# Optimization experiments

Hardware: AMD Instinct MI355X
Metric: run time of the kernel (lower is better)

## Reference

```python
import jax, jax.numpy as jnp
import numpy as np

BETA_MIN = 1e-06


def setup_inputs() -> dict:
    key = jax.random.key(0)
    ks = jax.random.split(key, 4)
    B, H, W, C = 32, 56, 56, 256
    x = jax.random.normal(ks[0], (B, H, W, C), dtype=jnp.float32)
    # NonNeg-constrained weights, init value gamma_init = 1/16
    gamma_k = jax.random.uniform(ks[1], (1, 1, 8, C), dtype=jnp.float32) * (1.0 / 16.0)
    gamma_s = jax.random.uniform(ks[2], (3, 3, C, 1), dtype=jnp.float32) * (1.0 / 16.0)
    beta = jax.random.uniform(ks[3], (C,), dtype=jnp.float32) * 1e-06
    beta_outside = jnp.zeros((C,), dtype=jnp.float32)
    gamma_outside = jnp.ones((C,), dtype=jnp.float32)
    return {
        'x': x,
        'gamma_k': gamma_k,
        'gamma_s': gamma_s,
        'beta': beta,
        'beta_outside': beta_outside,
        'gamma_outside': gamma_outside,
        'surround_dist': 1,
    }


def reference(x, gamma_k, gamma_s, beta, beta_outside, gamma_outside, surround_dist):
    B, H, W, C = x.shape
    G = C // 8  # norm_groups = C / 8, 8 channels per group

    x2 = x * x

    # Grouped 1x1 conv: gamma_k[0,0] is [8, C]; group g uses columns g*8:(g+1)*8
    # reshape to [in=8, group, out=8] and contract per group.
    w = gamma_k[0, 0].reshape(8, G, 8)  # [i, g, o]
    Pk = jnp.einsum('bhwgi,igo->bhwgo', x2.reshape(B, H, W, G, 8), w)
    Pk = Pk.reshape(B, H, W, C)

    # Masked (center-zero) dilated 3x3 depthwise conv on squared inputs.
    mask = jnp.array([[1.0, 1.0, 1.0], [1.0, 0.0, 1.0], [1.0, 1.0, 1.0]], dtype=x.dtype)
    k = gamma_s[..., 0] * mask[:, :, None]  # [3, 3, C]
    kern = k[:, :, None, :]  # HWIO with I = C/groups = 1, O = C
    Ps = jax.lax.conv_general_dilated(
        x2, kern,
        window_strides=(1, 1),
        padding='SAME',
        rhs_dilation=(surround_dist, surround_dist),
        dimension_numbers=('NHWC', 'HWIO', 'NHWC'),
        feature_group_count=C,
    )

    # Divisive normalization: x / sqrt(Pk + Ps + beta + beta_min), then affine.
    norm_pool = jnp.reciprocal(jnp.sqrt(Pk + Ps + (beta + BETA_MIN)))
    return x * norm_pool * gamma_outside + beta_outside
```

## Files before the change

kernel.cpp:

```cpp
#include <hip/hip_runtime.h>

#define BB 32
#define HH 56
#define WW 56
#define CC 256
#define PSTRIP 4
#define STRIPS_PER_ROW (WW / PSTRIP)

__device__ __forceinline__ void load8(const float* __restrict__ p, float v[8]) {
    float4 a = *reinterpret_cast<const float4*>(p);
    float4 b = *reinterpret_cast<const float4*>(p + 4);
    v[0]=a.x; v[1]=a.y; v[2]=a.z; v[3]=a.w;
    v[4]=b.x; v[5]=b.y; v[6]=b.z; v[7]=b.w;
}

__global__ __launch_bounds__(256, 2) void dn_kernel(
    const float* __restrict__ x,
    const float* __restrict__ gk_g,
    const float* __restrict__ gs_g,
    const float* __restrict__ beta,
    const float* __restrict__ beta_o,
    const float* __restrict__ gamma_o,
    const int* __restrict__ sdist,
    float* __restrict__ out)
{
    const int d   = sdist[0];
    const int tid = blockIdx.x * 256 + threadIdx.x;
    const int g   = tid & 31;
    const int s   = tid >> 5;
    const int sw  = s % STRIPS_PER_ROW;
    const int t1  = s / STRIPS_PER_ROW;
    const int h   = t1 % HH;
    const int b   = t1 / HH;
    const int w0  = sw * PSTRIP;
    const int c0  = g << 3;

    float gk[8][8];
#pragma unroll
    for (int i = 0; i < 8; ++i) load8(gk_g + i*CC + c0, gk[i]);

    const int tap_kh[8] = {0,0,0,1,1,2,2,2};
    const int tap_kw[8] = {0,1,2,0,2,0,1,2};
    float gs[8][8];
#pragma unroll
    for (int t = 0; t < 8; ++t)
        load8(gs_g + (tap_kh[t]*3 + tap_kw[t])*CC + c0, gs[t]);

    float betav[8], gov[8], bov[8];
    load8(beta    + c0, betav);
    load8(gamma_o + c0, gov);
    load8(beta_o  + c0, bov);
#pragma unroll
    for (int o = 0; o < 8; ++o) betav[o] += 1e-6f;

    const float* xrow = x   + (size_t)((b*HH + h)*WW)*CC;
    float*       orow = out + (size_t)((b*HH + h)*WW)*CC;

#pragma unroll
    for (int j = 0; j < PSTRIP; ++j) {
        const int w = w0 + j;

        float cx[8];
        load8(xrow + w*CC + c0, cx);

        float acc[8];
#pragma unroll
        for (int o = 0; o < 8; ++o) acc[o] = betav[o];

#pragma unroll
        for (int i = 0; i < 8; ++i) {
            const float x2 = cx[i]*cx[i];
#pragma unroll
            for (int o = 0; o < 8; ++o) acc[o] += x2 * gk[i][o];
        }

#pragma unroll
        for (int t = 0; t < 8; ++t) {
            const int hh = h + (tap_kh[t]-1)*d;
            const int w2 = w + (tap_kw[t]-1)*d;
            if (hh >= 0 && hh < HH && w2 >= 0 && w2 < WW) {
                float xn[8];
                load8(x + (size_t)((b*HH + hh)*WW + w2)*CC + c0, xn);
#pragma unroll
                for (int o = 0; o < 8; ++o) acc[o] += (xn[o]*xn[o]) * gs[t][o];
            }
        }

        float res[8];
#pragma unroll
        for (int o = 0; o < 8; ++o) {
            const float np = __builtin_amdgcn_rsqf(acc[o]);
            res[o] = cx[o] * np * gov[o] + bov[o];
        }
        float4* op = reinterpret_cast<float4*>(orow + w*CC + c0);
        op[0] = make_float4(res[0], res[1], res[2], res[3]);
        op[1] = make_float4(res[4], res[5], res[6], res[7]);
    }
}

extern "C" void kernel_launch(void* const* d_in, const int* in_sizes, int n_in,
                              void* d_out, int out_size, void* d_ws, size_t ws_size,
                              hipStream_t stream) {
    const float* x       = (const float*)d_in[0];
    const float* gamma_k = (const float*)d_in[1];
    const float* gamma_s = (const float*)d_in[2];
    const float* beta    = (const float*)d_in[3];
    const float* beta_o  = (const float*)d_in[4];
    const float* gamma_o = (const float*)d_in[5];
    const int*   sdist   = (const int*)d_in[6];
    float* out = (float*)d_out;

    const int total  = BB * HH * STRIPS_PER_ROW * 32;
    const int blocks = total / 256;
    dn_kernel<<<blocks, 256, 0, stream>>>(x, gamma_k, gamma_s, beta,
                                          beta_o, gamma_o, sdist, out);
}
```

Before: 267.1 us.

## Stage squared input tile with halo in LDS for depthwise and grouped conv

Each block now covers an 8-row by full-width spatial tile over 16 channels. It first loads the tile plus a one-pixel halo into shared memory, squared and with the float4 slots rotated to avoid bank conflicts. The 3x3 neighbour taps and the centre grouped 1x1 conv then read squared values from LDS instead of issuing 8 redundant global loads per pixel. Block indices are also remapped so that each XCD handles distinct batches, which is meant to improve L2 locality. The halo layout is sized for dilation 1, so larger surround_dist values would read outside the staged tile, and occupancy may be limited by the ~37KB LDS allocation.

```diff
diff --git a/kernel.cpp b/kernel.cpp
--- a/kernel.cpp
+++ b/kernel.cpp
@@ -1,20 +1,27 @@
 #include <hip/hip_runtime.h>
+
+typedef float floatx4 __attribute__((ext_vector_type(4)));
 
 #define BB 32
 #define HH 56
 #define WW 56
 #define CC 256
-#define PSTRIP 4
-#define STRIPS_PER_ROW (WW / PSTRIP)
+#define TILE_H 8
+#define HTILES 7
+#define CT 16
+#define CTILES 16
+#define SROWS (TILE_H + 2)
+#define SW (WW + 2)
+#define LDS_F4 (SROWS * SW * (CT/4))
 
 __device__ __forceinline__ void load8(const float* __restrict__ p, float v[8]) {
-    float4 a = *reinterpret_cast<const float4*>(p);
-    float4 b = *reinterpret_cast<const float4*>(p + 4);
-    v[0]=a.x; v[1]=a.y; v[2]=a.z; v[3]=a.w;
-    v[4]=b.x; v[5]=b.y; v[6]=b.z; v[7]=b.w;
+    floatx4 a = *reinterpret_cast<const floatx4*>(p);
+    floatx4 b = *reinterpret_cast<const floatx4*>(p + 4);
+    v[0]=a[0]; v[1]=a[1]; v[2]=a[2]; v[3]=a[3];
+    v[4]=b[0]; v[5]=b[1]; v[6]=b[2]; v[7]=b[3];
 }
 
-__global__ __launch_bounds__(256, 2) void dn_kernel(
+__global__ __launch_bounds__(128, 2) void dn_kernel(
     const float* __restrict__ x,
     const float* __restrict__ gk_g,
     const float* __restrict__ gs_g,
@@ -24,77 +31,119 @@
     const int* __restrict__ sdist,
     float* __restrict__ out)
 {
-    const int d   = sdist[0];
-    const int tid = blockIdx.x * 256 + threadIdx.x;
-    const int g   = tid & 31;
-    const int s   = tid >> 5;
-    const int sw  = s % STRIPS_PER_ROW;
-    const int t1  = s / STRIPS_PER_ROW;
-    const int h   = t1 % HH;
-    const int b   = t1 / HH;
-    const int w0  = sw * PSTRIP;
-    const int c0  = g << 3;
+    __shared__ float x2s[SROWS * SW * CT];
+
+    const int d = sdist[0];
+
+    const int xcd = blockIdx.x & 7;
+    const int q   = blockIdx.x >> 3;
+    const int b   = xcd + ((q / (HTILES*CTILES)) << 3);
+    const int t0  = q % (HTILES*CTILES);
+    const int htile = t0 >> 4;
+    const int ctile = t0 & 15;
+    const int h0 = htile * TILE_H;
+    const int c0 = ctile * CT;
+    const int tid = threadIdx.x;
+
+    const float* xb = x + (size_t)b * HH * WW * CC;
+
+    {
+        floatx4* ls = (floatx4*)x2s;
+        for (int s = tid; s < LDS_F4; s += 128) {
+            const int c4 = s & 3;
+            const int wp = (s >> 2) % SW;
+            const int r  = s / (SW * 4);
+            const int h  = h0 - 1 + r;
+            const int w  = wp - 1;
+            floatx4 v = {0.f, 0.f, 0.f, 0.f};
+            if ((unsigned)h < HH && (unsigned)w < WW) {
+                const int src4 = (c4 - wp) & 3;
+                const floatx4* gp = (const floatx4*)(xb + (size_t)(h*WW + w)*CC + c0) + src4;
+                floatx4 u = *gp;
+                v = u * u;
+            }
+            ls[s] = v;
+        }
+    }
+
+    const int row   = tid >> 4;
+    const int strip = (tid >> 1) & 7;
+    const int gi    = tid & 1;
+    const int cb    = c0 + gi * 8;
+    const int o4a   = gi * 2, o4b = gi * 2 + 1;
 
     float gk[8][8];
 #pragma unroll
-    for (int i = 0; i < 8; ++i) load8(gk_g + i*CC + c0, gk[i]);
+    for (int i = 0; i < 8; ++i) load8(gk_g + i*CC + cb, gk[i]);
 
     const int tap_kh[8] = {0,0,0,1,1,2,2,2};
     const int tap_kw[8] = {0,1,2,0,2,0,1,2};
     float gs[8][8];
 #pragma unroll
     for (int t = 0; t < 8; ++t)
-        load8(gs_g + (tap_kh[t]*3 + tap_kw[t])*CC + c0, gs[t]);
+        load8(gs_g + (tap_kh[t]*3 + tap_kw[t])*CC + cb, gs[t]);
 
     float betav[8], gov[8], bov[8];
-    load8(beta    + c0, betav);
-    load8(gamma_o + c0, gov);
-    load8(beta_o  + c0, bov);
+    load8(beta    + cb, betav);
+    load8(gamma_o + cb, gov);
+    load8(beta_o  + cb, bov);
 #pragma unroll
     for (int o = 0; o < 8; ++o) betav[o] += 1e-6f;
 
-    const float* xrow = x   + (size_t)((b*HH + h)*WW)*CC;
-    float*       orow = out + (size_t)((b*HH + h)*WW)*CC;
+    __syncthreads();
 
-#pragma unroll
-    for (int j = 0; j < PSTRIP; ++j) {
-        const int w = w0 + j;
+    const int h = h0 + row;
+    const float* xrow = xb + (size_t)(h * WW) * CC;
+    float*       orow = out + ((size_t)(b * HH + h) * WW) * CC;
+    const floatx4* ls = (const floatx4*)x2s;
+
+    for (int j = 0; j < 7; ++j) {
+        const int w  = strip * 7 + j;
+        const int wp = w + 1;
 
         float cx[8];
-        load8(xrow + w*CC + c0, cx);
+        load8(xrow + w*CC + cb, cx);
 
         float acc[8];
 #pragma unroll
         for (int o = 0; o < 8; ++o) acc[o] = betav[o];
 
+        int t = 0;
 #pragma unroll
-        for (int i = 0; i < 8; ++i) {
-            const float x2 = cx[i]*cx[i];
+        for (int dr = -1; dr <= 1; ++dr) {
 #pragma unroll
-            for (int o = 0; o < 8; ++o) acc[o] += x2 * gk[i][o];
-        }
-
+            for (int dw = -1; dw <= 1; ++dw) {
+                const int rt = row + 1 + dr * d;
+                const int wt = wp + dw * d;
+                const int fb = (rt * SW + wt) * (CT/4);
+                const floatx4 A = ls[fb + ((o4a + wt) & 3)];
+                const floatx4 B = ls[fb + ((o4b + wt) & 3)];
+                if (dr == 0 && dw == 0) {
 #pragma unroll
-        for (int t = 0; t < 8; ++t) {
-            const int hh = h + (tap_kh[t]-1)*d;
-            const int w2 = w + (tap_kw[t]-1)*d;
-            if (hh >= 0 && hh < HH && w2 >= 0 && w2 < WW) {
-                float xn[8];
-                load8(x + (size_t)((b*HH + hh)*WW + w2)*CC + c0, xn);
+                    for (int o = 0; o < 8; ++o)
+                        acc[o] += A[0]*gk[0][o] + A[1]*gk[1][o]
+                                + A[2]*gk[2][o] + A[3]*gk[3][o]
+                                + B[0]*gk[4][o] + B[1]*gk[5][o]
+                                + B[2]*gk[6][o] + B[3]*gk[7][o];
+                } else {
 #pragma unroll
-                for (int o = 0; o < 8; ++o) acc[o] += (xn[o]*xn[o]) * gs[t][o];
+                    for (int o = 0; o < 4; ++o) acc[o]     += A[o] * gs[t][o];
+#pragma unroll
+                    for (int o = 0; o < 4; ++o) acc[4 + o] += B[o] * gs[t][4 + o];
+                    ++t;
+                }
             }
         }
 
-        float res[8];
+        floatx4 r0, r1;
 #pragma unroll
-        for (int o = 0; o < 8; ++o) {
-            const float np = __builtin_amdgcn_rsqf(acc[o]);
-            res[o] = cx[o] * np * gov[o] + bov[o];
+        for (int o = 0; o < 4; ++o) {
+            r0[o] = cx[o]     * __builtin_amdgcn_rsqf(acc[o])     * gov[o]     + bov[o];
+            r1[o] = cx[4 + o] * __builtin_amdgcn_rsqf(acc[4 + o]) * gov[4 + o] + bov[4 + o];
         }
-        float4* op = reinterpret_cast<float4*>(orow + w*CC + c0);
-        op[0] = make_float4(res[0], res[1], res[2], res[3]);
-        op[1] = make_float4(res[4], res[5], res[6], res[7]);
+        floatx4* op = (floatx4*)(orow + w*CC + cb);
+        op[0] = r0;
+        op[1] = r1;
     }
 }
 
@@ -110,8 +159,7 @@
     const int*   sdist   = (const int*)d_in[6];
     float* out = (float*)d_out;
 
-    const int total  = BB * HH * STRIPS_PER_ROW * 32;
-    const int blocks = total / 256;
-    dn_kernel<<<blocks, 256, 0, stream>>>(x, gamma_k, gamma_s, beta,
+    const int blocks = BB * HTILES * CTILES;
+    dn_kernel<<<blocks, 128, 0, stream>>>(x, gamma_k, gamma_s, beta,
                                           beta_o, gamma_o, sdist, out);
 }
```

After: 245.3 us. 8.2% less time.

## Remap threads to 4 channels each with 2D tiles and XCD-aware block mapping

Applied to the files above, without the earlier changes.

Each thread now computes 4 output channels instead of 8, so a wavefront covers a full pixel's 256 channels and a block covers a 4-row by 4-column tile. Block indices are swizzled so that each XCD works on its own images, which should improve L2 reuse of the neighbouring halo rows. The change also loads all neighbour taps before the math, uses nontemporal stores for the output and raises the occupancy hint. The trade-off is that the grouped 1x1 conv now reads the group's 8 inputs redundantly in pairs of lanes.

```diff
diff --git a/kernel.cpp b/kernel.cpp
--- a/kernel.cpp
+++ b/kernel.cpp
@@ -1,20 +1,18 @@
 #include <hip/hip_runtime.h>
+
+typedef float floatx4 __attribute__((ext_vector_type(4)));
 
 #define BB 32
 #define HH 56
 #define WW 56
 #define CC 256
 #define PSTRIP 4
-#define STRIPS_PER_ROW (WW / PSTRIP)
+#define WSTRIPS 14
+#define HTILE 4
+#define HTILES 14
+#define BLOCKS_PER_IMG (HTILES * WSTRIPS)
 
-__device__ __forceinline__ void load8(const float* __restrict__ p, float v[8]) {
-    float4 a = *reinterpret_cast<const float4*>(p);
-    float4 b = *reinterpret_cast<const float4*>(p + 4);
-    v[0]=a.x; v[1]=a.y; v[2]=a.z; v[3]=a.w;
-    v[4]=b.x; v[5]=b.y; v[6]=b.z; v[7]=b.w;
-}
-
-__global__ __launch_bounds__(256, 2) void dn_kernel(
+__global__ __launch_bounds__(256, 3) void dn_kernel(
     const float* __restrict__ x,
     const float* __restrict__ gk_g,
     const float* __restrict__ gs_g,
@@ -24,77 +22,77 @@
     const int* __restrict__ sdist,
     float* __restrict__ out)
 {
-    const int d   = sdist[0];
-    const int tid = blockIdx.x * 256 + threadIdx.x;
-    const int g   = tid & 31;
-    const int s   = tid >> 5;
-    const int sw  = s % STRIPS_PER_ROW;
-    const int t1  = s / STRIPS_PER_ROW;
-    const int h   = t1 % HH;
-    const int b   = t1 / HH;
-    const int w0  = sw * PSTRIP;
-    const int c0  = g << 3;
-
-    float gk[8][8];
-#pragma unroll
-    for (int i = 0; i < 8; ++i) load8(gk_g + i*CC + c0, gk[i]);
+    const int d    = sdist[0];
+    const int xcd  = blockIdx.x & 7;
+    const int q    = blockIdx.x >> 3;
+    const int b    = xcd + ((q / BLOCKS_PER_IMG) << 3);
+    const int t0   = q % BLOCKS_PER_IMG;
+    const int h    = (t0 / WSTRIPS) * HTILE + (threadIdx.x >> 6);
+    const int w0   = (t0 % WSTRIPS) * PSTRIP;
+    const int lane = threadIdx.x & 63;
+    const int c0   = lane << 2;
+    const int cg   = c0 & ~7;
 
     const int tap_kh[8] = {0,0,0,1,1,2,2,2};
     const int tap_kw[8] = {0,1,2,0,2,0,1,2};
-    float gs[8][8];
+
+    floatx4 gk[8];
 #pragma unroll
-    for (int t = 0; t < 8; ++t)
-        load8(gs_g + (tap_kh[t]*3 + tap_kw[t])*CC + c0, gs[t]);
+    for (int i = 0; i < 8; ++i)
+        gk[i] = *reinterpret_cast<const floatx4*>(gk_g + i*CC + c0);
 
-    float betav[8], gov[8], bov[8];
-    load8(beta    + c0, betav);
-    load8(gamma_o + c0, gov);
-    load8(beta_o  + c0, bov);
+    floatx4 gsw[8];
 #pragma unroll
-    for (int o = 0; o < 8; ++o) betav[o] += 1e-6f;
+    for (int tt = 0; tt < 8; ++tt)
+        gsw[tt] = *reinterpret_cast<const floatx4*>(
+                      gs_g + (tap_kh[tt]*3 + tap_kw[tt])*CC + c0);
 
-    const float* xrow = x   + (size_t)((b*HH + h)*WW)*CC;
-    float*       orow = out + (size_t)((b*HH + h)*WW)*CC;
+    floatx4 betav = *reinterpret_cast<const floatx4*>(beta + c0);
+    betav += 1e-6f;
+    const floatx4 gov = *reinterpret_cast<const floatx4*>(gamma_o + c0);
+    const floatx4 bov = *reinterpret_cast<const floatx4*>(beta_o  + c0);
+
+    const float* xb   = x + (size_t)b * HH * WW * CC;
+    const float* xrow = xb + (size_t)h * WW * CC;
+    float*       orow = out + ((size_t)(b*HH + h) * WW) * CC;
 
 #pragma unroll
     for (int j = 0; j < PSTRIP; ++j) {
         const int w = w0 + j;
+        const float* cp = xrow + w*CC;
 
-        float cx[8];
-        load8(xrow + w*CC + c0, cx);
+        floatx4 cxa = *reinterpret_cast<const floatx4*>(cp + cg);
+        floatx4 cxb = *reinterpret_cast<const floatx4*>(cp + cg + 4);
 
-        float acc[8];
+        floatx4 tp[8];
 #pragma unroll
-        for (int o = 0; o < 8; ++o) acc[o] = betav[o];
-
-#pragma unroll
-        for (int i = 0; i < 8; ++i) {
-            const float x2 = cx[i]*cx[i];
-#pragma unroll
-            for (int o = 0; o < 8; ++o) acc[o] += x2 * gk[i][o];
+        for (int tt = 0; tt < 8; ++tt) {
+            const int hh = h + (tap_kh[tt]-1)*d;
+            const int w2 = w + (tap_kw[tt]-1)*d;
+            floatx4 v = {0.f, 0.f, 0.f, 0.f};
+            if ((unsigned)hh < HH && (unsigned)w2 < WW)
+                v = *reinterpret_cast<const floatx4*>(
+                        xb + (size_t)(hh*WW + w2)*CC + c0);
+            tp[tt] = v;
         }
 
+        floatx4 acc = betav;
+        const floatx4 sqa = cxa*cxa, sqb = cxb*cxb;
 #pragma unroll
-        for (int t = 0; t < 8; ++t) {
-            const int hh = h + (tap_kh[t]-1)*d;
-            const int w2 = w + (tap_kw[t]-1)*d;
-            if (hh >= 0 && hh < HH && w2 >= 0 && w2 < WW) {
-                float xn[8];
-                load8(x + (size_t)((b*HH + hh)*WW + w2)*CC + c0, xn);
+        for (int i = 0; i < 4; ++i) acc += sqa[i] * gk[i];
 #pragma unroll
-                for (int o = 0; o < 8; ++o) acc[o] += (xn[o]*xn[o]) * gs[t][o];
-            }
-        }
+        for (int i = 0; i < 4; ++i) acc += sqb[i] * gk[4+i];
+#pragma unroll
+        for (int tt = 0; tt < 8; ++tt) acc += (tp[tt]*tp[tt]) * gsw[tt];
 
-        float res[8];
+        const floatx4 cxo = (lane & 1) ? cxb : cxa;
+        floatx4 res;
 #pragma unroll
-        for (int o = 0; o < 8; ++o) {
-            const float np = __builtin_amdgcn_rsqf(acc[o]);
-            res[o] = cx[o] * np * gov[o] + bov[o];
-        }
-        float4* op = reinterpret_cast<float4*>(orow + w*CC + c0);
-        op[0] = make_float4(res[0], res[1], res[2], res[3]);
-        op[1] = make_float4(res[4], res[5], res[6], res[7]);
+        for (int o = 0; o < 4; ++o)
+            res[o] = cxo[o] * __builtin_amdgcn_rsqf(acc[o]) * gov[o] + bov[o];
+
+        __builtin_nontemporal_store(res,
+            reinterpret_cast<floatx4*>(orow + w*CC + c0));
     }
 }
 
@@ -110,8 +108,7 @@
     const int*   sdist   = (const int*)d_in[6];
     float* out = (float*)d_out;
 
-    const int total  = BB * HH * STRIPS_PER_ROW * 32;
-    const int blocks = total / 256;
+    const int blocks = BB * BLOCKS_PER_IMG;
     dn_kernel<<<blocks, 256, 0, stream>>>(x, gamma_k, gamma_s, beta,
                                           beta_o, gamma_o, sdist, out);
 }
```

After: 241.2 us. -9.7%, faster.
